# Optimization experiments

Hardware: AMD Instinct MI355X
Metric: run time of the kernel (lower is better)

## Reference

```python
import jax, jax.numpy as jnp
import numpy as np

N_NODES = 100000
N_EDGES = 1600000
D_IN, D_HID, D_OUT = 512, 256, 40
DROPOUT_P = 0.5


def setup_inputs() -> dict:
    key = jax.random.key(0)
    ks = jax.random.split(key, 8)
    x = jax.random.normal(ks[0], (N_NODES, D_IN), dtype=jnp.float32)
    edge_src = jax.random.randint(ks[1], (N_EDGES,), 0, N_NODES, dtype=jnp.int32)
    edge_dst = jax.random.randint(ks[2], (N_EDGES,), 0, N_NODES, dtype=jnp.int32)
    edge_weight = jax.random.uniform(ks[3], (N_EDGES,), dtype=jnp.float32)
    W1 = jax.random.normal(ks[4], (D_IN, D_HID), dtype=jnp.float32) * (1.0 / np.sqrt(D_IN))
    b1 = jax.random.normal(ks[5], (D_HID,), dtype=jnp.float32) * 0.01
    W2 = jax.random.normal(ks[6], (D_HID, D_OUT), dtype=jnp.float32) * (1.0 / np.sqrt(D_HID))
    b2 = jax.random.normal(ks[7], (D_OUT,), dtype=jnp.float32) * 0.01
    return {"x": x, "edge_src": edge_src, "edge_dst": edge_dst, "edge_weight": edge_weight,
            "W1": W1, "b1": b1, "W2": W2, "b2": b2}


def _graph_conv(x, src, dst, ew, W, b):
    # support = x @ W  (dense GEMM), then spmm: out[d] = sum_e ew[e] * support[src[e]]
    support = x @ W                                  # [N, F_out]
    msgs = support[src] * ew[:, None]                # [E, F_out] gather + scale
    return jax.ops.segment_sum(msgs, dst, num_segments=N_NODES) + b


def reference(x, edge_src, edge_dst, edge_weight, W1, b1, W2, b2):
    h = jax.nn.relu(_graph_conv(x, edge_src, edge_dst, edge_weight, W1, b1))
    # dropout (train mode, fixed key for determinism), inverted scaling
    keep = jax.random.bernoulli(jax.random.key(42), 1.0 - DROPOUT_P, h.shape)
    h = jnp.where(keep, h / (1.0 - DROPOUT_P), 0.0)
    logits = _graph_conv(h, edge_src, edge_dst, edge_weight, W2, b2)
    return jax.nn.log_softmax(logits, axis=1)
```

## Files before the change

kernel.cpp:

```cpp
#include <hip/hip_runtime.h>
#include <hip/hip_bf16.h>
#include <math.h>

#define N_NODES 100000
#define N_EDGES 1600000
#define D_IN 512
#define D_HID 256
#define D_OUT 40
#define S2_LD 48
#define SCAN_BLOCKS ((N_NODES + 255) / 256)
#define NSHADOW 8

#define G1_BLOCKS ((N_NODES + 127) / 128)
#define HIST_BLOCKS ((N_EDGES + 511) / 512)
#define W2T_N (48 * D_HID)
#define W2T_BLOCKS ((W2T_N + 511) / 512)

typedef short short8 __attribute__((ext_vector_type(8)));
typedef short short4v __attribute__((ext_vector_type(4)));
typedef float f32x4 __attribute__((ext_vector_type(4)));

static __device__ __forceinline__ short f2bf(float f) {
  union { __hip_bfloat16 b; short s; } u;
  u.b = __float2bfloat16(f);
  return u.s;
}
static __device__ __forceinline__ float bf2f(unsigned short h) {
  return __uint_as_float(((unsigned)h) << 16);
}

static __device__ __forceinline__ void threefry_0_42(unsigned x0, unsigned x1,
                                                     unsigned& o0, unsigned& o1) {
  const unsigned ks0 = 0u;
  const unsigned ks1 = 42u;
  const unsigned ks2 = 0u ^ 42u ^ 0x1BD11BDAu;
  x0 += ks0; x1 += ks1;
#define TF_R(r) { x0 += x1; x1 = (x1 << (r)) | (x1 >> (32 - (r))); x1 ^= x0; }
  TF_R(13) TF_R(15) TF_R(26) TF_R(6)
  x0 += ks1; x1 += ks2 + 1u;
  TF_R(17) TF_R(29) TF_R(16) TF_R(24)
  x0 += ks2; x1 += ks0 + 2u;
  TF_R(13) TF_R(15) TF_R(26) TF_R(6)
  x0 += ks0; x1 += ks1 + 3u;
  TF_R(17) TF_R(29) TF_R(16) TF_R(24)
  x0 += ks1; x1 += ks2 + 4u;
  TF_R(13) TF_R(15) TF_R(26) TF_R(6)
  x0 += ks2; x1 += ks0 + 5u;
#undef TF_R
  o0 = x0; o1 = x1;
}

__global__ __launch_bounds__(512) void w1t_only_kernel(const float* __restrict__ W1,
                                                       short* __restrict__ W1t) {
  const int i = blockIdx.x * 512 + threadIdx.x;
  if (i >= D_IN * D_HID) return;
  const int n = i >> 9;
  const int k = i & 511;
  W1t[i] = f2bf(W1[(size_t)k * D_HID + n]);
}

__global__ __launch_bounds__(256) void block_sum_kernel(const int* __restrict__ counts8,
                                                        int* __restrict__ counts_tot,
                                                        int* __restrict__ bsums) {
  __shared__ int red[256];
  const int t = threadIdx.x;
  const int i = blockIdx.x * 256 + t;
  int c = 0;
  if (i < N_NODES) {
#pragma unroll
    for (int s = 0; s < NSHADOW; ++s) c += counts8[s * N_NODES + i];
    counts_tot[i] = c;
  }
  red[t] = c;
  __syncthreads();
#pragma unroll
  for (int off = 128; off > 0; off >>= 1) {
    if (t < off) red[t] += red[t + off];
    __syncthreads();
  }
  if (t == 0) bsums[blockIdx.x] = red[0];
}

__global__ __launch_bounds__(512) void bsum_scan_kernel(const int* __restrict__ bsums,
                                                        int* __restrict__ boffs) {
  __shared__ int tmp[512];
  const int t = threadIdx.x;
  const int v = (t < SCAN_BLOCKS) ? bsums[t] : 0;
  tmp[t] = v;
  __syncthreads();
  for (int off = 1; off < 512; off <<= 1) {
    const int add = (t >= off) ? tmp[t - off] : 0;
    __syncthreads();
    tmp[t] += add;
    __syncthreads();
  }
  if (t < SCAN_BLOCKS) boffs[t] = tmp[t] - v;
}

__global__ __launch_bounds__(256) void scan_apply_kernel(const int* __restrict__ counts_tot,
                                                         const int* __restrict__ boffs,
                                                         int* __restrict__ rowptr,
                                                         int* __restrict__ cursor) {
  __shared__ int tmp[256];
  const int t = threadIdx.x;
  const int i = blockIdx.x * 256 + t;
  const int v = (i < N_NODES) ? counts_tot[i] : 0;
  tmp[t] = v;
  __syncthreads();
  for (int off = 1; off < 256; off <<= 1) {
    const int add = (t >= off) ? tmp[t - off] : 0;
    __syncthreads();
    tmp[t] += add;
    __syncthreads();
  }
  const int excl = boffs[blockIdx.x] + tmp[t] - v;
  if (i < N_NODES) {
    rowptr[i] = excl;
    cursor[i] = excl;
    if (i == N_NODES - 1) rowptr[N_NODES] = excl + v;
  }
}

__global__ __launch_bounds__(256) void scatter_kernel(const int* __restrict__ esrc,
                                                      const int* __restrict__ edst,
                                                      const float* __restrict__ ew,
                                                      int* __restrict__ cursor,
                                                      int2* __restrict__ pairs) {
  const int e = blockIdx.x * 256 + threadIdx.x;
  if (e >= N_EDGES) return;
  const int d = edst[e];
  const int pos = atomicAdd(&cursor[d], 1);
  int2 p;
  p.x = esrc[e];
  p.y = __float_as_int(ew[e]);
  pairs[pos] = p;
}

__global__ __launch_bounds__(512) void k1_gemm1_hist_w2t_kernel(
    const float* __restrict__ x, const short* __restrict__ W1t,
    short* __restrict__ out,
    const int* __restrict__ edst, int* __restrict__ counts8,
    const float* __restrict__ W2, short* __restrict__ W2t) {
  const int bid = blockIdx.x;
  const int tid = threadIdx.x;

  if (bid >= G1_BLOCKS) {
    const int xb = bid - G1_BLOCKS;
    if (xb < HIST_BLOCKS) {
      const int e = xb * 512 + tid;
      if (e < N_EDGES) atomicAdd(&counts8[(xb & 7) * N_NODES + edst[e]], 1);
    } else {
      const int j = (xb - HIST_BLOCKS) * 512 + tid;
      if (j < W2T_N) {
        const int n = j >> 8;
        const int k = j & 255;
        W2t[j] = (n < D_OUT) ? f2bf(W2[(size_t)k * D_OUT + n]) : (short)0;
      }
    }
    return;
  }

  __shared__ __attribute__((aligned(16))) short As[128][40];
  __shared__ __attribute__((aligned(16))) short Bs[256][40];

  const int lane = tid & 63;
  const int wid  = tid >> 6;
  const int wm   = wid >> 2;
  const int wn   = wid & 3;
  const int lr   = lane & 15;
  const int lg   = lane >> 4;
  const int row0 = bid * 128;

  f32x4 acc[4][4] = {};

  for (int kt = 0; kt < D_IN; kt += 32) {
    {
      const int m  = tid >> 2;
      const int kc = tid & 3;
      short8 v;
      const int grow = row0 + m;
      if (grow < N_NODES) {
        const float* src = x + (size_t)grow * D_IN + kt + kc * 8;
        const float4 f0 = *(const float4*)(src);
        const float4 f1 = *(const float4*)(src + 4);
        v[0] = f2bf(f0.x); v[1] = f2bf(f0.y); v[2] = f2bf(f0.z); v[3] = f2bf(f0.w);
        v[4] = f2bf(f1.x); v[5] = f2bf(f1.y); v[6] = f2bf(f1.z); v[7] = f2bf(f1.w);
      } else {
        v = (short8)0;
      }
      *(short8*)&As[m][kc * 8] = v;
    }
    {
#pragma unroll
      for (int c = 0; c < 2; ++c) {
        const int t2 = (tid << 1) | c;
        const int n  = t2 >> 2;
        const int kc = t2 & 3;
        const short8 v = *(const short8*)(W1t + (size_t)n * D_IN + kt + kc * 8);
        *(short8*)&Bs[n][kc * 8] = v;
      }
    }
    __syncthreads();

    short8 a[4], b[4];
#pragma unroll
    for (int mi = 0; mi < 4; ++mi)
      a[mi] = *(const short8*)&As[wm * 64 + mi * 16 + lr][lg * 8];
#pragma unroll
    for (int nj = 0; nj < 4; ++nj)
      b[nj] = *(const short8*)&Bs[wn * 64 + nj * 16 + lr][lg * 8];

#pragma unroll
    for (int mi = 0; mi < 4; ++mi)
#pragma unroll
      for (int nj = 0; nj < 4; ++nj)
        acc[mi][nj] = __builtin_amdgcn_mfma_f32_16x16x32_bf16(a[mi], b[nj], acc[mi][nj], 0, 0, 0);

    __syncthreads();
  }

#pragma unroll
  for (int mi = 0; mi < 4; ++mi) {
#pragma unroll
    for (int nj = 0; nj < 4; ++nj) {
      const int gcol = wn * 64 + nj * 16 + lr;
#pragma unroll
      for (int r = 0; r < 4; ++r) {
        const int grow = row0 + wm * 64 + mi * 16 + lg * 4 + r;
        if (grow < N_NODES) out[(size_t)grow * D_HID + gcol] = f2bf(acc[mi][nj][r]);
      }
    }
  }
}

__global__ __launch_bounds__(256) void spmm1_csr_kernel(const short* __restrict__ sup,
                                                        const int* __restrict__ rowptr,
                                                        const int2* __restrict__ pairs,
                                                        const float* __restrict__ b1,
                                                        short* __restrict__ h) {
  const int node = blockIdx.x * 4 + (threadIdx.x >> 6);
  const int lane = threadIdx.x & 63;
  const int half = lane >> 5;
  const int hl   = lane & 31;
  if (node >= N_NODES) return;
  const int beg = rowptr[node];
  const int end = rowptr[node + 1];

  float acc[8] = {};

  int e = beg + half;
  for (; e + 6 < end; e += 8) {
    const int2 p0 = pairs[e];
    const int2 p1 = pairs[e + 2];
    const int2 p2 = pairs[e + 4];
    const int2 p3 = pairs[e + 6];
    const short8 v0 = *(const short8*)(sup + (size_t)p0.x * D_HID + hl * 8);
    const short8 v1 = *(const short8*)(sup + (size_t)p1.x * D_HID + hl * 8);
    const short8 v2 = *(const short8*)(sup + (size_t)p2.x * D_HID + hl * 8);
    const short8 v3 = *(const short8*)(sup + (size_t)p3.x * D_HID + hl * 8);
    const float w0 = __int_as_float(p0.y);
    const float w1 = __int_as_float(p1.y);
    const float w2 = __int_as_float(p2.y);
    const float w3 = __int_as_float(p3.y);
#pragma unroll
    for (int j = 0; j < 8; ++j) acc[j] += w0 * bf2f((unsigned short)v0[j]);
#pragma unroll
    for (int j = 0; j < 8; ++j) acc[j] += w1 * bf2f((unsigned short)v1[j]);
#pragma unroll
    for (int j = 0; j < 8; ++j) acc[j] += w2 * bf2f((unsigned short)v2[j]);
#pragma unroll
    for (int j = 0; j < 8; ++j) acc[j] += w3 * bf2f((unsigned short)v3[j]);
  }
  for (; e < end; e += 2) {
    const int2 p0 = pairs[e];
    const float w0 = __int_as_float(p0.y);
    const short8 v0 = *(const short8*)(sup + (size_t)p0.x * D_HID + hl * 8);
#pragma unroll
    for (int j = 0; j < 8; ++j) acc[j] += w0 * bf2f((unsigned short)v0[j]);
  }

#pragma unroll
  for (int j = 0; j < 8; ++j) acc[j] += __shfl_xor(acc[j], 32, 64);

  const int col = hl * 8 + half * 4;
  short4v r;
#pragma unroll
  for (int j = 0; j < 4; ++j) {
    float v = acc[half * 4 + j] + b1[col + j];
    v = v > 0.0f ? v : 0.0f;
    unsigned o0, o1;
    threefry_0_42(0u, (unsigned)node * D_HID + col + j, o0, o1);
    const unsigned word = o0 ^ o1;
    r[j] = (word >> 31) ? (short)0 : f2bf(v * 2.0f);
  }
  *(short4v*)(h + (size_t)node * D_HID + col) = r;
}

__global__ __launch_bounds__(256) void gemm2_mfma_kernel(const short* __restrict__ h,
                                                         const short* __restrict__ W2t,
                                                         short* __restrict__ out) {
  __shared__ __attribute__((aligned(16))) short As[128][40];
  __shared__ __attribute__((aligned(16))) short Bs[48][40];

  const int tid  = threadIdx.x;
  const int lane = tid & 63;
  const int wm   = tid >> 6;
  const int lr   = lane & 15;
  const int lg   = lane >> 4;
  const int row0 = blockIdx.x * 128;

  f32x4 acc[2][3] = {};

  for (int kt = 0; kt < D_HID; kt += 32) {
    {
#pragma unroll
      for (int c = 0; c < 2; ++c) {
        const int t2 = (tid << 1) | c;
        const int m  = t2 >> 2;
        const int kc = t2 & 3;
        const int grow = row0 + m;
        short8 v = (short8)0;
        if (grow < N_NODES)
          v = *(const short8*)(h + (size_t)grow * D_HID + kt + kc * 8);
        *(short8*)&As[m][kc * 8] = v;
      }
    }
    if (tid < 192) {
      const int n  = tid >> 2;
      const int kc = tid & 3;
      const short8 v = *(const short8*)(W2t + (size_t)n * D_HID + kt + kc * 8);
      *(short8*)&Bs[n][kc * 8] = v;
    }
    __syncthreads();

    short8 a[2], b[3];
#pragma unroll
    for (int mi = 0; mi < 2; ++mi)
      a[mi] = *(const short8*)&As[wm * 32 + mi * 16 + lr][lg * 8];
#pragma unroll
    for (int nj = 0; nj < 3; ++nj)
      b[nj] = *(const short8*)&Bs[nj * 16 + lr][lg * 8];

#pragma unroll
    for (int mi = 0; mi < 2; ++mi)
#pragma unroll
      for (int nj = 0; nj < 3; ++nj)
        acc[mi][nj] = __builtin_amdgcn_mfma_f32_16x16x32_bf16(a[mi], b[nj], acc[mi][nj], 0, 0, 0);

    __syncthreads();
  }

#pragma unroll
  for (int mi = 0; mi < 2; ++mi) {
#pragma unroll
    for (int nj = 0; nj < 3; ++nj) {
      const int gcol = nj * 16 + lr;
      if (gcol < D_OUT) {
#pragma unroll
        for (int r = 0; r < 4; ++r) {
          const int grow = row0 + wm * 32 + mi * 16 + lg * 4 + r;
          if (grow < N_NODES) out[(size_t)grow * S2_LD + gcol] = f2bf(acc[mi][nj][r]);
        }
      }
    }
  }
}

__global__ __launch_bounds__(256) void spmm2_csr_kernel(const short* __restrict__ sup2,
                                                        const int* __restrict__ rowptr,
                                                        const int2* __restrict__ pairs,
                                                        const float* __restrict__ b2,
                                                        float* __restrict__ out) {
  const int lane = threadIdx.x & 63;
  const int half = lane >> 5;
  const int hl   = lane & 31;
  const int node = blockIdx.x * 8 + ((threadIdx.x >> 6) << 1) + half;
  if (node >= N_NODES) return;
  const int beg = rowptr[node];
  const int end = rowptr[node + 1];
  const bool act = hl < 20;

  float a0 = 0.f, a1 = 0.f, b0 = 0.f, b1 = 0.f;
  float c0 = 0.f, c1 = 0.f, d0 = 0.f, d1 = 0.f;
  int e = beg;
  for (; e + 4 <= end; e += 4) {
    const int2 p0 = pairs[e], p1 = pairs[e + 1], p2 = pairs[e + 2], p3 = pairs[e + 3];
    if (act) {
      const unsigned u0 = *(const unsigned*)(sup2 + (size_t)p0.x * S2_LD + hl * 2);
      const unsigned u1 = *(const unsigned*)(sup2 + (size_t)p1.x * S2_LD + hl * 2);
      const unsigned u2 = *(const unsigned*)(sup2 + (size_t)p2.x * S2_LD + hl * 2);
      const unsigned u3 = *(const unsigned*)(sup2 + (size_t)p3.x * S2_LD + hl * 2);
      const float w0 = __int_as_float(p0.y);
      const float w1 = __int_as_float(p1.y);
      const float w2 = __int_as_float(p2.y);
      const float w3 = __int_as_float(p3.y);
      a0 += w0 * bf2f((unsigned short)(u0 & 0xffff)); a1 += w0 * bf2f((unsigned short)(u0 >> 16));
      b0 += w1 * bf2f((unsigned short)(u1 & 0xffff)); b1 += w1 * bf2f((unsigned short)(u1 >> 16));
      c0 += w2 * bf2f((unsigned short)(u2 & 0xffff)); c1 += w2 * bf2f((unsigned short)(u2 >> 16));
      d0 += w3 * bf2f((unsigned short)(u3 & 0xffff)); d1 += w3 * bf2f((unsigned short)(u3 >> 16));
    }
  }
  for (; e < end; ++e) {
    const int2 p0 = pairs[e];
    if (act) {
      const unsigned u0 = *(const unsigned*)(sup2 + (size_t)p0.x * S2_LD + hl * 2);
      const float w0 = __int_as_float(p0.y);
      a0 += w0 * bf2f((unsigned short)(u0 & 0xffff)); a1 += w0 * bf2f((unsigned short)(u0 >> 16));
    }
  }
  const float f0 = (a0 + b0) + (c0 + d0);
  const float f1 = (a1 + b1) + (c1 + d1);

  const float v0 = act ? f0 + b2[hl * 2]     : -INFINITY;
  const float v1 = act ? f1 + b2[hl * 2 + 1] : -INFINITY;
  float m = fmaxf(v0, v1);
#pragma unroll
  for (int off = 16; off > 0; off >>= 1) m = fmaxf(m, __shfl_xor(m, off, 32));
  float s = act ? __expf(v0 - m) + __expf(v1 - m) : 0.0f;
#pragma unroll
  for (int off = 16; off > 0; off >>= 1) s += __shfl_xor(s, off, 32);
  if (act) {
    const float ls = logf(s);
    float2 r;
    r.x = v0 - m - ls;
    r.y = v1 - m - ls;
    *(float2*)&out[(size_t)node * D_OUT + hl * 2] = r;
  }
}

extern "C" void kernel_launch(void* const* d_in, const int* in_sizes, int n_in,
                              void* d_out, int out_size, void* d_ws, size_t ws_size,
                              hipStream_t stream) {
  const float* x    = (const float*)d_in[0];
  const int*   esrc = (const int*)d_in[1];
  const int*   edst = (const int*)d_in[2];
  const float* ew   = (const float*)d_in[3];
  const float* W1   = (const float*)d_in[4];
  const float* b1   = (const float*)d_in[5];
  const float* W2   = (const float*)d_in[6];
  const float* b2   = (const float*)d_in[7];
  float* out = (float*)d_out;

  float* ws = (float*)d_ws;
  short* support1 = (short*)ws;
  short* hbuf     = (short*)(ws + 12800000);
  short* support2 = (short*)(ws + 25600000);
  int2*  pairs    = (int2*)(ws + 30400000);
  int*   rowptr   = (int*)(ws + 33600000);
  int*   counts_t = (int*)(ws + 33700008);
  int*   cursor   = (int*)(ws + 33800008);
  short* W1t      = (short*)(ws + 33900008);
  short* W2t      = (short*)(ws + 33965544);
  int*   bsums    = (int*)(ws + 33971688);
  int*   boffs    = bsums + 512;
  int*   counts8  = (int*)(ws + 33972712);

  hipMemsetAsync(counts8, 0, (size_t)NSHADOW * N_NODES * sizeof(int), stream);

  w1t_only_kernel<<<(D_IN * D_HID + 511) / 512, 512, 0, stream>>>(W1, W1t);

  k1_gemm1_hist_w2t_kernel<<<G1_BLOCKS + HIST_BLOCKS + W2T_BLOCKS, 512, 0, stream>>>(
      x, W1t, support1, edst, counts8, W2, W2t);

  block_sum_kernel<<<SCAN_BLOCKS, 256, 0, stream>>>(counts8, counts_t, bsums);
  bsum_scan_kernel<<<1, 512, 0, stream>>>(bsums, boffs);
  scan_apply_kernel<<<SCAN_BLOCKS, 256, 0, stream>>>(counts_t, boffs, rowptr, cursor);
  scatter_kernel<<<(N_EDGES + 255) / 256, 256, 0, stream>>>(esrc, edst, ew, cursor, pairs);

  spmm1_csr_kernel<<<(N_NODES + 3) / 4, 256, 0, stream>>>(support1, rowptr, pairs, b1, hbuf);

  gemm2_mfma_kernel<<<(N_NODES + 127) / 128, 256, 0, stream>>>(hbuf, W2t, support2);
  spmm2_csr_kernel<<<(N_NODES + 7) / 8, 256, 0, stream>>>(support2, rowptr, pairs, b2, out);
}
```

Baseline: 436.7 us.

## Pre-convert x to bf16 and fuse GEMM1 with edge scatter kernel

Moves the fp32-to-bf16 conversion of x into a separate prep kernel that also does the histogram and both weight transposes. GEMM1 now reads bf16 x with 64-row tiles and 256 threads, and is launched together with the CSR scatter blocks so the two can overlap; the W1t and W2t transposes share one launch. The cost is an extra write and read of a 100 MB bf16 copy of x and a larger workspace, and GEMM1 reloads the W1 tile twice as often per row.

```diff
diff --git a/kernel.cpp b/kernel.cpp
--- a/kernel.cpp
+++ b/kernel.cpp
@@ -11,12 +11,16 @@
 #define SCAN_BLOCKS ((N_NODES + 255) / 256)
 #define NSHADOW 8
 
-#define G1_BLOCKS ((N_NODES + 127) / 128)
+#define XCONV_BLOCKS 12500
 #define HIST_BLOCKS ((N_EDGES + 511) / 512)
-#define W2T_N (48 * D_HID)
-#define W2T_BLOCKS ((W2T_N + 511) / 512)
+#define W1T_BLOCKS 256
+#define W2T_BLOCKS 24
+
+#define G1_BLOCKS ((N_NODES + 63) / 64)
+#define SCAT_BLOCKS ((N_EDGES + 255) / 256)
 
 typedef short short8 __attribute__((ext_vector_type(8)));
+typedef short short16 __attribute__((ext_vector_type(16)));
 typedef short short4v __attribute__((ext_vector_type(4)));
 typedef float f32x4 __attribute__((ext_vector_type(4)));
 
@@ -50,13 +54,47 @@
   o0 = x0; o1 = x1;
 }
 
-__global__ __launch_bounds__(512) void w1t_only_kernel(const float* __restrict__ W1,
-                                                       short* __restrict__ W1t) {
-  const int i = blockIdx.x * 512 + threadIdx.x;
-  if (i >= D_IN * D_HID) return;
-  const int n = i >> 9;
-  const int k = i & 511;
-  W1t[i] = f2bf(W1[(size_t)k * D_HID + n]);
+__global__ __launch_bounds__(512) void prep_kernel(
+    const float* __restrict__ x, short* __restrict__ xb,
+    const int* __restrict__ edst, int* __restrict__ counts8,
+    const float* __restrict__ W1, short* __restrict__ W1t,
+    const float* __restrict__ W2, short* __restrict__ W2t) {
+  const int bid = blockIdx.x;
+  const int tid = threadIdx.x;
+
+  if (bid < XCONV_BLOCKS) {
+    const size_t i0 = ((size_t)bid * 512 + tid) * 8;
+    const float4 f0 = *(const float4*)(x + i0);
+    const float4 f1 = *(const float4*)(x + i0 + 4);
+    short8 v;
+    v[0] = f2bf(f0.x); v[1] = f2bf(f0.y); v[2] = f2bf(f0.z); v[3] = f2bf(f0.w);
+    v[4] = f2bf(f1.x); v[5] = f2bf(f1.y); v[6] = f2bf(f1.z); v[7] = f2bf(f1.w);
+    *(short8*)(xb + i0) = v;
+    return;
+  }
+  int xb2 = bid - XCONV_BLOCKS;
+  if (xb2 < HIST_BLOCKS) {
+    const int e = xb2 * 512 + tid;
+    if (e < N_EDGES) atomicAdd(&counts8[(xb2 & 7) * N_NODES + edst[e]], 1);
+    return;
+  }
+  xb2 -= HIST_BLOCKS;
+  if (xb2 < W1T_BLOCKS) {
+    const int i = xb2 * 512 + tid;
+    const int n = i >> 9;
+    const int k = i & 511;
+    W1t[i] = f2bf(W1[(size_t)k * D_HID + n]);
+    return;
+  }
+  xb2 -= W1T_BLOCKS;
+  {
+    const int j = xb2 * 512 + tid;
+    if (j < 48 * D_HID) {
+      const int n = j >> 8;
+      const int k = j & 255;
+      W2t[j] = (n < D_OUT) ? f2bf(W2[(size_t)k * D_OUT + n]) : (short)0;
+    }
+  }
 }
 
 __global__ __launch_bounds__(256) void block_sum_kernel(const int* __restrict__ counts8,
@@ -121,55 +159,36 @@
   }
 }
 
-__global__ __launch_bounds__(256) void scatter_kernel(const int* __restrict__ esrc,
-                                                      const int* __restrict__ edst,
-                                                      const float* __restrict__ ew,
-                                                      int* __restrict__ cursor,
-                                                      int2* __restrict__ pairs) {
-  const int e = blockIdx.x * 256 + threadIdx.x;
-  if (e >= N_EDGES) return;
-  const int d = edst[e];
-  const int pos = atomicAdd(&cursor[d], 1);
-  int2 p;
-  p.x = esrc[e];
-  p.y = __float_as_int(ew[e]);
-  pairs[pos] = p;
-}
-
-__global__ __launch_bounds__(512) void k1_gemm1_hist_w2t_kernel(
-    const float* __restrict__ x, const short* __restrict__ W1t,
+__global__ __launch_bounds__(256) void gemm1_scatter_kernel(
+    const short* __restrict__ xb, const short* __restrict__ W1t,
     short* __restrict__ out,
-    const int* __restrict__ edst, int* __restrict__ counts8,
-    const float* __restrict__ W2, short* __restrict__ W2t) {
+    const int* __restrict__ esrc, const int* __restrict__ edst,
+    const float* __restrict__ ew, int* __restrict__ cursor,
+    int2* __restrict__ pairs) {
   const int bid = blockIdx.x;
   const int tid = threadIdx.x;
 
   if (bid >= G1_BLOCKS) {
-    const int xb = bid - G1_BLOCKS;
-    if (xb < HIST_BLOCKS) {
-      const int e = xb * 512 + tid;
-      if (e < N_EDGES) atomicAdd(&counts8[(xb & 7) * N_NODES + edst[e]], 1);
-    } else {
-      const int j = (xb - HIST_BLOCKS) * 512 + tid;
-      if (j < W2T_N) {
-        const int n = j >> 8;
-        const int k = j & 255;
-        W2t[j] = (n < D_OUT) ? f2bf(W2[(size_t)k * D_OUT + n]) : (short)0;
-      }
+    const int e = (bid - G1_BLOCKS) * 256 + tid;
+    if (e < N_EDGES) {
+      const int d = edst[e];
+      const int pos = atomicAdd(&cursor[d], 1);
+      int2 p;
+      p.x = esrc[e];
+      p.y = __float_as_int(ew[e]);
+      pairs[pos] = p;
     }
     return;
   }
 
-  __shared__ __attribute__((aligned(16))) short As[128][40];
+  __shared__ __attribute__((aligned(16))) short As[64][40];
   __shared__ __attribute__((aligned(16))) short Bs[256][40];
 
   const int lane = tid & 63;
-  const int wid  = tid >> 6;
-  const int wm   = wid >> 2;
-  const int wn   = wid & 3;
+  const int wn   = tid >> 6;
   const int lr   = lane & 15;
   const int lg   = lane >> 4;
-  const int row0 = bid * 128;
+  const int row0 = bid * 64;
 
   f32x4 acc[4][4] = {};
 
@@ -177,35 +196,25 @@
     {
       const int m  = tid >> 2;
       const int kc = tid & 3;
-      short8 v;
       const int grow = row0 + m;
-      if (grow < N_NODES) {
-        const float* src = x + (size_t)grow * D_IN + kt + kc * 8;
-        const float4 f0 = *(const float4*)(src);
-        const float4 f1 = *(const float4*)(src + 4);
-        v[0] = f2bf(f0.x); v[1] = f2bf(f0.y); v[2] = f2bf(f0.z); v[3] = f2bf(f0.w);
-        v[4] = f2bf(f1.x); v[5] = f2bf(f1.y); v[6] = f2bf(f1.z); v[7] = f2bf(f1.w);
-      } else {
-        v = (short8)0;
-      }
+      short8 v = (short8)0;
+      if (grow < N_NODES)
+        v = *(const short8*)(xb + (size_t)grow * D_IN + kt + kc * 8);
       *(short8*)&As[m][kc * 8] = v;
     }
     {
-#pragma unroll
-      for (int c = 0; c < 2; ++c) {
-        const int t2 = (tid << 1) | c;
-        const int n  = t2 >> 2;
-        const int kc = t2 & 3;
-        const short8 v = *(const short8*)(W1t + (size_t)n * D_IN + kt + kc * 8);
-        *(short8*)&Bs[n][kc * 8] = v;
-      }
+      const short* bs = W1t + (size_t)tid * D_IN + kt;
+      const short16 b0 = *(const short16*)(bs);
+      const short16 b1 = *(const short16*)(bs + 16);
+      *(short16*)&Bs[tid][0]  = b0;
+      *(short16*)&Bs[tid][16] = b1;
     }
     __syncthreads();
 
     short8 a[4], b[4];
 #pragma unroll
     for (int mi = 0; mi < 4; ++mi)
-      a[mi] = *(const short8*)&As[wm * 64 + mi * 16 + lr][lg * 8];
+      a[mi] = *(const short8*)&As[mi * 16 + lr][lg * 8];
 #pragma unroll
     for (int nj = 0; nj < 4; ++nj)
       b[nj] = *(const short8*)&Bs[wn * 64 + nj * 16 + lr][lg * 8];
@@ -226,7 +235,7 @@
       const int gcol = wn * 64 + nj * 16 + lr;
 #pragma unroll
       for (int r = 0; r < 4; ++r) {
-        const int grow = row0 + wm * 64 + mi * 16 + lg * 4 + r;
+        const int grow = row0 + mi * 16 + lg * 4 + r;
         if (grow < N_NODES) out[(size_t)grow * D_HID + gcol] = f2bf(acc[mi][nj][r]);
       }
     }
@@ -443,29 +452,30 @@
 
   float* ws = (float*)d_ws;
   short* support1 = (short*)ws;
-  short* hbuf     = (short*)(ws + 12800000);
-  short* support2 = (short*)(ws + 25600000);
-  int2*  pairs    = (int2*)(ws + 30400000);
-  int*   rowptr   = (int*)(ws + 33600000);
-  int*   counts_t = (int*)(ws + 33700008);
-  int*   cursor   = (int*)(ws + 33800008);
-  short* W1t      = (short*)(ws + 33900008);
-  short* W2t      = (short*)(ws + 33965544);
-  int*   bsums    = (int*)(ws + 33971688);
+  short* xb       = (short*)(ws + 12800000);
+  short* hbuf     = xb;
+  short* support2 = (short*)(ws + 38400000);
+  int2*  pairs    = (int2*)(ws + 40800000);
+  int*   rowptr   = (int*)(ws + 44000000);
+  int*   counts_t = (int*)(ws + 44100008);
+  int*   cursor   = (int*)(ws + 44200008);
+  short* W1t      = (short*)(ws + 44300008);
+  short* W2t      = (short*)(ws + 44365544);
+  int*   bsums    = (int*)(ws + 44371688);
   int*   boffs    = bsums + 512;
-  int*   counts8  = (int*)(ws + 33972712);
+  int*   counts8  = (int*)(ws + 44372712);
 
   hipMemsetAsync(counts8, 0, (size_t)NSHADOW * N_NODES * sizeof(int), stream);
 
-  w1t_only_kernel<<<(D_IN * D_HID + 511) / 512, 512, 0, stream>>>(W1, W1t);
-
-  k1_gemm1_hist_w2t_kernel<<<G1_BLOCKS + HIST_BLOCKS + W2T_BLOCKS, 512, 0, stream>>>(
-      x, W1t, support1, edst, counts8, W2, W2t);
+  prep_kernel<<<XCONV_BLOCKS + HIST_BLOCKS + W1T_BLOCKS + W2T_BLOCKS, 512, 0, stream>>>(
+      x, xb, edst, counts8, W1, W1t, W2, W2t);
 
   block_sum_kernel<<<SCAN_BLOCKS, 256, 0, stream>>>(counts8, counts_t, bsums);
   bsum_scan_kernel<<<1, 512, 0, stream>>>(bsums, boffs);
   scan_apply_kernel<<<SCAN_BLOCKS, 256, 0, stream>>>(counts_t, boffs, rowptr, cursor);
-  scatter_kernel<<<(N_EDGES + 255) / 256, 256, 0, stream>>>(esrc, edst, ew, cursor, pairs);
+
+  gemm1_scatter_kernel<<<G1_BLOCKS + SCAT_BLOCKS, 256, 0, stream>>>(
+      xb, W1t, support1, esrc, edst, ew, cursor, pairs);
 
   spmm1_csr_kernel<<<(N_NODES + 3) / 4, 256, 0, stream>>>(support1, rowptr, pairs, b1, hbuf);
 
```

After: 488.6 us. 11.9% more time.
